# Performance work log

Hardware: AMD Instinct MI355X
Metric: run time of the kernel (lower is better)

The kernel has to match this reference:

```python
import jax, jax.numpy as jnp
import numpy as np

L, H, S, HID, E, TOPK = 2, 8, 1024, 512, 8, 2
FFN = 2 * HID
EPS = 1e-5


def setup_inputs() -> dict:
    key = jax.random.key(0)
    ks = jax.random.split(key, 20)
    B = 4
    sc = 0.02
    inp = {
        'x': jax.random.normal(ks[0], (B, S, HID), jnp.float32),
        'encoder_output': jax.random.normal(ks[1], (B, S, HID), jnp.float32),
        # two attentions per layer -> axis 1 of size 2 (0: masked self-attn, 1: cross-attn)
        'attn_wq': jax.random.normal(ks[2], (L, 2, HID, H * HID), jnp.float32) * sc,
        'attn_bq': jnp.zeros((L, 2, H * HID), jnp.float32),
        'attn_wk': jax.random.normal(ks[3], (L, 2, HID, H * HID), jnp.float32) * sc,
        'attn_bk': jnp.zeros((L, 2, H * HID), jnp.float32),
        'attn_wv': jax.random.normal(ks[4], (L, 2, HID, H * HID), jnp.float32) * sc,
        'attn_bv': jnp.zeros((L, 2, H * HID), jnp.float32),
        'attn_wo': jax.random.normal(ks[5], (L, 2, H * HID, HID), jnp.float32) * sc,
        'attn_bo': jnp.zeros((L, 2, HID), jnp.float32),
        'gate_w': jax.random.normal(ks[6], (L, HID, E), jnp.float32) * sc,
        'gate_b': jnp.zeros((L, E), jnp.float32),
        'exp_w1': jax.random.normal(ks[7], (L, E, HID, FFN), jnp.float32) * sc,
        'exp_b1': jnp.zeros((L, E, FFN), jnp.float32),
        'exp_w2': jax.random.normal(ks[8], (L, E, FFN, HID), jnp.float32) * sc,
        'exp_b2': jnp.zeros((L, E, HID), jnp.float32),
        'ln_g': jnp.ones((L, 3, HID), jnp.float32),
        'ln_b': jnp.zeros((L, 3, HID), jnp.float32),
    }
    return inp


def _layernorm(x, g, b):
    m = jnp.mean(x, -1, keepdims=True)
    v = jnp.mean(jnp.square(x - m), -1, keepdims=True)
    return g * (x - m) * jax.lax.rsqrt(v + EPS) + b


def _mha(q_in, k_in, v_in, wq, bq, wk, bk, wv, bv, wo, bo, masked):
    B = q_in.shape[0]
    # torch .view(-1, H, S, h) on [B, S, H*h]: raw memory reshape (faithful quirk)
    q = (q_in @ wq + bq).reshape(B, H, S, HID)
    k = (k_in @ wk + bk).reshape(B, H, S, HID)
    v = (v_in @ wv + bv).reshape(B, H, S, HID)
    scores = jnp.einsum('bhqd,bhkd->bhqk', q, k)  # d_k=1 -> scale = 1.0
    if masked:
        causal = jnp.triu(jnp.ones((S, S), jnp.float32), k=1)
        scores = jnp.where(causal == 1, -jnp.inf, scores)
    attn = jax.nn.softmax(scores, axis=-1)  # dropout off (eval)
    out = jnp.einsum('bhqk,bhkd->bhqd', attn, v)
    out = out.transpose(0, 2, 1, 3).reshape(B, S, H * HID)
    return out @ wo + bo


def _moe(x, gw, gb, w1, b1, w2, b2):
    gate = jax.nn.softmax(x @ gw + gb, axis=-1)  # [B,S,E]
    topw, topi = jax.lax.top_k(gate, TOPK)
    topw = topw / jnp.sum(topw, -1, keepdims=True)
    # faithful bug: the torch loop overwrites, so only k = TOPK-1 survives
    sel = topi[..., TOPK - 1]  # [B,S]
    wsel = topw[..., TOPK - 1]  # [B,S]
    y = jnp.zeros_like(x)
    for e in range(E):
        he = jax.nn.relu(x @ w1[e] + b1[e]) @ w2[e] + b2[e]
        y = y + jnp.where((sel == e)[..., None], he, 0.0)
    return y * wsel[..., None]


def reference(x, encoder_output, attn_wq, attn_bq, attn_wk, attn_bk, attn_wv,
              attn_bv, attn_wo, attn_bo, gate_w, gate_b, exp_w1, exp_b1,
              exp_w2, exp_b2, ln_g, ln_b):
    for l in range(L):
        a = _mha(x, x, x,
                 attn_wq[l, 0], attn_bq[l, 0], attn_wk[l, 0], attn_bk[l, 0],
                 attn_wv[l, 0], attn_bv[l, 0], attn_wo[l, 0], attn_bo[l, 0],
                 masked=True)
        x = _layernorm(a + x, ln_g[l, 0], ln_b[l, 0])
        # cross-attn: query & key from encoder, values from x (faithful to source)
        a2 = _mha(encoder_output, encoder_output, x,
                  attn_wq[l, 1], attn_bq[l, 1], attn_wk[l, 1], attn_bk[l, 1],
                  attn_wv[l, 1], attn_bv[l, 1], attn_wo[l, 1], attn_bo[l, 1],
                  masked=False)
        x = _layernorm(x + a2, ln_g[l, 1], ln_b[l, 1])
        f = _moe(x, gate_w[l], gate_b[l], exp_w1[l], exp_b1[l], exp_w2[l], exp_b2[l])
        x = _layernorm(x + f, ln_g[l, 2], ln_b[l, 2])
    return x
```

## Files before the change

### kernel.cpp

```cpp
#include <hip/hip_runtime.h>
#include <math.h>


typedef unsigned short bf16_t;
typedef __attribute__((ext_vector_type(8))) short s16x8;
typedef __attribute__((ext_vector_type(8))) unsigned short u16x8;
typedef __attribute__((ext_vector_type(4))) float f32x4;

__device__ __forceinline__ float bf2f(bf16_t u) {
    union { unsigned int i; float f; } v; v.i = ((unsigned int)u) << 16; return v.f;
}
__device__ __forceinline__ bf16_t f2bf(float f) {
    union { float f; unsigned int i; } v; v.f = f;
    unsigned int x = v.i;
    return (bf16_t)((x + 0x7fffu + ((x >> 16) & 1u)) >> 16);
}
__device__ __forceinline__ bf16_t bfhi_trunc(float x, float& rem) {
    union { float f; unsigned u; } v; v.f = x;
    unsigned hu = v.u & 0xFFFF0000u;
    union { unsigned u; float f; } h; h.u = hu;
    rem = x - h.f;
    return (bf16_t)(hu >> 16);
}

__device__ __forceinline__ float waveReduceSum(float x) {
    x += __shfl_xor(x, 1);  x += __shfl_xor(x, 2);  x += __shfl_xor(x, 4);
    x += __shfl_xor(x, 8);  x += __shfl_xor(x, 16); x += __shfl_xor(x, 32);
    return x;
}
__device__ __forceinline__ float waveReduceMax(float x) {
    x = fmaxf(x, __shfl_xor(x, 1));  x = fmaxf(x, __shfl_xor(x, 2));
    x = fmaxf(x, __shfl_xor(x, 4));  x = fmaxf(x, __shfl_xor(x, 8));
    x = fmaxf(x, __shfl_xor(x, 16)); x = fmaxf(x, __shfl_xor(x, 32));
    return x;
}

__global__ void probe_kernel(const unsigned int* __restrict__ lng_u32,
                             int* __restrict__ flag)
{
    if (threadIdx.x == 0 && blockIdx.x == 0)
        *flag = (lng_u32[0] == 0x3F803F80u) ? 1 : 0;
}


__device__ __forceinline__ void stage_f32_row(const float* __restrict__ src,
                                              char* rowp, int h, int r)
{
    float xx[16];
    *(float4*)(xx + 0)  = *(const float4*)(src + 0);
    *(float4*)(xx + 4)  = *(const float4*)(src + 4);
    *(float4*)(xx + 8)  = *(const float4*)(src + 8);
    *(float4*)(xx + 12) = *(const float4*)(src + 12);
    u16x8 h0, h1, l0, l1;
#pragma unroll
    for (int i = 0; i < 8; i++) {
        float r0, r1;
        h0[i] = bfhi_trunc(xx[i], r0);      l0[i] = f2bf(r0);
        h1[i] = bfhi_trunc(xx[8 + i], r1);  l1[i] = f2bf(r1);
    }
    const int sw = (r & 7) << 4;
    *(u16x8*)(rowp + ((32 * h + 0)  ^ sw)) = h0;
    *(u16x8*)(rowp + ((32 * h + 16) ^ sw)) = h1;
    *(u16x8*)(rowp + ((64 + 32 * h + 0)  ^ sw)) = l0;
    *(u16x8*)(rowp + ((64 + 32 * h + 16) ^ sw)) = l1;
}

__device__ __forceinline__ void stage_bf16_row(const bf16_t* __restrict__ src,
                                               char* rowp, int h, int r)
{
    u16x8 v0 = *(const u16x8*)(src);
    u16x8 v1 = *(const u16x8*)(src + 8);
    const int sw = (r & 7) << 4;
    *(u16x8*)(rowp + ((32 * h + 0)  ^ sw)) = v0;
    *(u16x8*)(rowp + ((32 * h + 16) ^ sw)) = v1;
}

__device__ __forceinline__ void stage_wnn_bf16(const bf16_t* __restrict__ src,
                                               int ldb, ushort (*Bs)[64],
                                               int kp2, int n8)
{
    u16x8 r0 = *(const u16x8*)(src);
    u16x8 r1 = *(const u16x8*)(src + ldb);
#pragma unroll
    for (int j = 0; j < 8; j++) {
        int rr = n8 + j;
        unsigned v = (unsigned)(unsigned short)r0[j] |
                     ((unsigned)(unsigned short)r1[j] << 16);
        *(unsigned*)((char*)&Bs[rr][0] + ((2 * kp2) ^ ((rr & 7) << 4))) = v;
    }
}

__device__ __forceinline__ void stage_wnn_f32(const float* __restrict__ src,
                                              int ldb, ushort (*Bs)[64],
                                              int kp2, int n8)
{
    float a0[8], a1[8];
    *(float4*)(a0 + 0) = *(const float4*)(src);
    *(float4*)(a0 + 4) = *(const float4*)(src + 4);
    *(float4*)(a1 + 0) = *(const float4*)(src + ldb);
    *(float4*)(a1 + 4) = *(const float4*)(src + ldb + 4);
#pragma unroll
    for (int j = 0; j < 8; j++) {
        int rr = n8 + j;
        float q0, q1;
        bf16_t h0 = bfhi_trunc(a0[j], q0);
        bf16_t h1 = bfhi_trunc(a1[j], q1);
        unsigned vh = (unsigned)h0 | ((unsigned)h1 << 16);
        unsigned vl = (unsigned)f2bf(q0) | ((unsigned)f2bf(q1) << 16);
        char* rp = (char*)&Bs[rr][0];
        int sw = (rr & 7) << 4;
        *(unsigned*)(rp + ((2 * kp2) ^ sw)) = vh;
        *(unsigned*)(rp + ((64 + 2 * kp2) ^ sw)) = vl;
    }
}

template<bool NT, bool RELU, bool GATHER, bool SCALE>
__device__ __forceinline__
void mgemm_body(const float* __restrict__ aF, const bf16_t* __restrict__ aH,
                const bool aBf,
                const float* __restrict__ bF, const bf16_t* __restrict__ bH,
                const bool bBf,
                const float* __restrict__ biasF, const bf16_t* __restrict__ biasH,
                const bool bf, const bool hasb,
                float* __restrict__ Cp,
                int lda, int ldb, int ldc,
                int Meff, const int* __restrict__ gl,
                const float* __restrict__ scalev,
                int kBeg, int kEnd, int m0, int n0)
{
    __shared__ __align__(16) ushort As[128][64];
    __shared__ __align__(16) ushort Bs[128][64];

    const int t   = threadIdx.x;
    const int sr  = t >> 1;
    const int sh  = t & 1;
    const int kp2 = (t & 15) * 2;
    const int n8  = (t >> 4) * 8;

    int agr = m0 + sr;
    if (GATHER) agr = gl[(m0 + sr < Meff) ? (m0 + sr) : (Meff - 1)];

    const int lane = t & 63;
    const int wv = t >> 6;
    const int wr = wv >> 1, wc = wv & 1;
    const int lr = lane & 15, kg = lane >> 4;

    int aoffH[4], aoffL[4], boffH[4], boffL[4];
#pragma unroll
    for (int i = 0; i < 4; i++) {
        int ra = wr * 64 + i * 16 + lr;
        int sa = (ra & 7) << 4;
        aoffH[i] = ra * 128 + ((kg * 16) ^ sa);
        aoffL[i] = ra * 128 + ((64 + kg * 16) ^ sa);
        int rb = wc * 64 + i * 16 + lr;
        int sb = (rb & 7) << 4;
        boffH[i] = rb * 128 + ((kg * 16) ^ sb);
        boffL[i] = rb * 128 + ((64 + kg * 16) ^ sb);
    }

    f32x4 acc[4][4];
#pragma unroll
    for (int i = 0; i < 4; i++)
#pragma unroll
        for (int j = 0; j < 4; j++)
            acc[i][j] = (f32x4){0.f, 0.f, 0.f, 0.f};

    for (int k0 = kBeg; k0 < kEnd; k0 += 32) {
        __syncthreads();
        {
            char* rowp = (char*)&As[sr][0];
            if (aBf) stage_bf16_row(aH + (long)agr * lda + k0 + sh * 16, rowp, sh, sr);
            else     stage_f32_row (aF + (long)agr * lda + k0 + sh * 16, rowp, sh, sr);
        }
        if (NT) {
            char* rowp = (char*)&Bs[sr][0];
            stage_f32_row(bF + (long)(n0 + sr) * ldb + k0 + sh * 16, rowp, sh, sr);
        } else if (bBf) {
            stage_wnn_bf16(bH + (long)(k0 + kp2) * ldb + n0 + n8, ldb, Bs, kp2, n8);
        } else {
            stage_wnn_f32 (bF + (long)(k0 + kp2) * ldb + n0 + n8, ldb, Bs, kp2, n8);
        }
        __syncthreads();

        s16x8 aHi[4], aLo[4];
#pragma unroll
        for (int i = 0; i < 4; i++)
            aHi[i] = *(const s16x8*)((const char*)As + aoffH[i]);
        if (!aBf) {
#pragma unroll
            for (int i = 0; i < 4; i++)
                aLo[i] = *(const s16x8*)((const char*)As + aoffL[i]);
        }

#pragma unroll
        for (int j = 0; j < 4; j++) {
            s16x8 bHi = *(const s16x8*)((const char*)Bs + boffH[j]);
#pragma unroll
            for (int i = 0; i < 4; i++)
                acc[i][j] = __builtin_amdgcn_mfma_f32_16x16x32_bf16(
                    aHi[i], bHi, acc[i][j], 0, 0, 0);
            if (!bBf) {
                s16x8 bLo = *(const s16x8*)((const char*)Bs + boffL[j]);
#pragma unroll
                for (int i = 0; i < 4; i++)
                    acc[i][j] = __builtin_amdgcn_mfma_f32_16x16x32_bf16(
                        aHi[i], bLo, acc[i][j], 0, 0, 0);
            }
            if (!aBf) {
#pragma unroll
                for (int i = 0; i < 4; i++)
                    acc[i][j] = __builtin_amdgcn_mfma_f32_16x16x32_bf16(
                        aLo[i], bHi, acc[i][j], 0, 0, 0);
            }
        }
    }

#pragma unroll
    for (int j = 0; j < 4; j++) {
        int col = n0 + wc * 64 + j * 16 + lr;
        float bv = 0.f;
        if (hasb) bv = bf ? bf2f(biasH[col]) : biasF[col];
#pragma unroll
        for (int i = 0; i < 4; i++) {
#pragma unroll
            for (int rr = 0; rr < 4; rr++) {
                int grow = m0 + wr * 64 + i * 16 + kg * 4 + rr;
                if (GATHER && grow >= Meff) continue;
                int crow = GATHER ? gl[grow] : grow;
                float v = acc[i][j][rr] + bv;
                if (RELU) v = fmaxf(v, 0.f);
                if (SCALE) v *= scalev[crow];
                Cp[(long)crow * ldc + col] = v;
            }
        }
    }
}

template<bool A_INPUT, bool B_WEIGHT, bool NT, bool RELU, bool GATHER,
         bool SCALE, bool MASK_TRI, bool MASK_K, bool SPLITK>
__global__ __launch_bounds__(256, 2)
void mgemm_kernel(const void* a32, const void* a16,
                  const void* b32, const void* b16,
                  const void* bias32, const void* bias16,
                  float* __restrict__ C,
                  int M, int N, int K, int lda, int ldb, int ldc,
                  long aZ, long bZ, long biasZ, long cZ,
                  const int* __restrict__ glist, const int* __restrict__ counts,
                  const float* __restrict__ scalev,
                  const int* __restrict__ dtf)
{
    if (MASK_TRI && blockIdx.x > blockIdx.y) return;
    const int e  = SPLITK ? 0 : blockIdx.z;
    const int n0 = blockIdx.x * 128, m0 = blockIdx.y * 128;
    int Meff = M;
    const int* gl = nullptr;
    if (GATHER) {
        gl = glist + e * 4096;
        Meff = counts[e];
        if (m0 >= Meff) return;
    }
    const bool bf  = (*dtf != 0);
    const bool aBf = A_INPUT && bf;
    const bool bBf = B_WEIGHT && bf;

    const float*  aF = (const float*)a32 + (long)e * aZ;
    const bf16_t* aH = (const bf16_t*)a16 + (long)e * aZ;
    const long bOff  = SPLITK ? 0 : (long)e * bZ;
    const float*  bF = (const float*)b32 + bOff;
    const bf16_t* bH = (const bf16_t*)b16 + bOff;

    float* Cp;
    int kBeg = 0, kEnd = K;
    if (SPLITK) {
        const int kc  = blockIdx.z;
        const int kch = (int)bZ;
        kBeg = kc * kch;
        kEnd = kBeg + kch;
        Cp = C + (long)kc * cZ;
    } else {
        Cp = C + (long)e * cZ;
        if (MASK_K) kEnd = (blockIdx.y + 1) * 128;
    }
    const bool hasb = !SPLITK && ((bias32 != nullptr) || (bias16 != nullptr));
    const float*  biasF = (const float*)bias32 + (long)e * biasZ;
    const bf16_t* biasH = (const bf16_t*)bias16 + (long)e * biasZ;

    mgemm_body<NT, RELU, GATHER, SCALE>(aF, aH, aBf, bF, bH, bBf,
        biasF, biasH, bf, hasb, Cp, lda, ldb, ldc, Meff, gl, scalev,
        kBeg, kEnd, m0, n0);
}

struct TriArgs {
    const void* a32[3]; const void* a16[3];
    const void* w32[3]; const void* w16[3];
    const void* b32[3]; const void* b16[3];
    float* dst[3];
    int aIn[3];
};

__global__ __launch_bounds__(256, 2)
void mgemm_tri_kernel(TriArgs ta, int lda, int ldb, int ldc, int K,
                      const int* __restrict__ dtf)
{
    const int z  = blockIdx.z;
    const int n0 = blockIdx.x * 128, m0 = blockIdx.y * 128;
    const bool bf  = (*dtf != 0);
    const bool aBf = (ta.aIn[z] != 0) && bf;
    mgemm_body<false, false, false, false>(
        (const float*)ta.a32[z], (const bf16_t*)ta.a16[z], aBf,
        (const float*)ta.w32[z], (const bf16_t*)ta.w16[z], bf,
        (const float*)ta.b32[z], (const bf16_t*)ta.b16[z], bf, true,
        ta.dst[z], lda, ldb, ldc, 0, nullptr, nullptr,
        0, K, m0, n0);
}

template<int NCH>
__global__ __launch_bounds__(256)
void reduce_kernel(const float* __restrict__ part,
                   const void* bias32, const void* bias16,
                   float* __restrict__ out, const int* __restrict__ dtf)
{
    const bool bf = (*dtf != 0);
    const int i = (blockIdx.x * 256 + threadIdx.x) * 4;
    float4 s = *(const float4*)(part + i);
#pragma unroll
    for (int c = 1; c < NCH; c++) {
        float4 p = *(const float4*)(part + (long)c * 524288 + i);
        s.x += p.x; s.y += p.y; s.z += p.z; s.w += p.w;
    }
    const int col = i & 511;
    float b0, b1, b2, b3;
    if (bf) {
        const bf16_t* bb = (const bf16_t*)bias16;
        b0 = bf2f(bb[col]); b1 = bf2f(bb[col + 1]);
        b2 = bf2f(bb[col + 2]); b3 = bf2f(bb[col + 3]);
    } else {
        const float* bb = (const float*)bias32;
        b0 = bb[col]; b1 = bb[col + 1]; b2 = bb[col + 2]; b3 = bb[col + 3];
    }
    out[i + 0] = s.x + b0; out[i + 1] = s.y + b1;
    out[i + 2] = s.z + b2; out[i + 3] = s.w + b3;
}

template<bool MASKED>
__global__ __launch_bounds__(256)
void softmax_kernel(float* __restrict__ sb)
{
    const int g = blockIdx.x * 4 + (threadIdx.x >> 6);
    const int lane = threadIdx.x & 63;
    const int r = g & 1023;
    float* row = sb + (long)g * 1024;
    const int n = MASKED ? (r + 1) : 1024;

    float vv[16];
    float m = -1e30f;
#pragma unroll
    for (int j = 0; j < 4; j++) {
        float4 v4 = *(const float4*)(row + j * 256 + lane * 4);
        const float* pv = (const float*)&v4;
#pragma unroll
        for (int c = 0; c < 4; c++) {
            int idx = j * 256 + lane * 4 + c;
            float x = (idx < n) ? pv[c] : -1e30f;
            vv[j * 4 + c] = x;
            m = fmaxf(m, x);
        }
    }
    m = waveReduceMax(m);
    float sum = 0.0f;
#pragma unroll
    for (int i = 0; i < 16; i++) {
        vv[i] = __expf(vv[i] - m);
        sum += vv[i];
    }
    sum = waveReduceSum(sum);
    float inv = 1.0f / sum;
#pragma unroll
    for (int j = 0; j < 4; j++) {
        float4 o = make_float4(vv[j * 4 + 0] * inv, vv[j * 4 + 1] * inv,
                               vv[j * 4 + 2] * inv, vv[j * 4 + 3] * inv);
        *(float4*)(row + j * 256 + lane * 4) = o;
    }
}

template<bool MASKED>
__global__ __launch_bounds__(256)
void flash_kernel(const float* __restrict__ q, const float* __restrict__ k,
                  const float* __restrict__ v, float* __restrict__ outc)
{
    const int h = blockIdx.y;
    const long bh = (long)h * 524288L;
    q += bh; k += bh; v += bh;
    const int t = threadIdx.x, lane = t & 63, wave = t >> 6;
    const int base = blockIdx.x * 32;
    const int row0 = base + wave * 8;

    float qreg[8][8], oacc[8][8];
    float mi[8], li[8];
#pragma unroll
    for (int i = 0; i < 8; i++) {
        mi[i] = -1e30f;
        li[i] = 0.0f;
#pragma unroll
        for (int d = 0; d < 8; d++) {
            qreg[i][d] = q[(long)(row0 + i) * 512 + lane + 64 * d];
            oacc[i][d] = 0.0f;
        }
    }

    __shared__ float ks[8][512];
    __shared__ float vs[8][512];

    const int kmax = MASKED ? (base + 31) : 1023;
    for (int k0 = 0; k0 <= kmax; k0 += 8) {
        __syncthreads();
#pragma unroll
        for (int r = 0; r < 4; r++) {
            int flat = (r * 256 + t) * 4;
            int kr = flat >> 9, col = flat & 511;
            *(float4*)&ks[kr][col] = *(const float4*)&k[(long)(k0 + kr) * 512 + col];
            *(float4*)&vs[kr][col] = *(const float4*)&v[(long)(k0 + kr) * 512 + col];
        }
        __syncthreads();
#pragma unroll
        for (int j = 0; j < 8; j++) {
            const int kg = k0 + j;
#pragma unroll
            for (int i = 0; i < 8; i++) {
                const int qrow = row0 + i;
                if (MASKED && kg > qrow) continue;
                float p = 0.0f;
#pragma unroll
                for (int d = 0; d < 8; d++)
                    p = fmaf(qreg[i][d], ks[j][lane + 64 * d], p);
                p = waveReduceSum(p);
                float mnew = fmaxf(mi[i], p);
                float sc = __expf(mi[i] - mnew);
                float pe = __expf(p - mnew);
                li[i] = li[i] * sc + pe;
                mi[i] = mnew;
#pragma unroll
                for (int d = 0; d < 8; d++)
                    oacc[i][d] = fmaf(oacc[i][d], sc, pe * vs[j][lane + 64 * d]);
            }
        }
    }

#pragma unroll
    for (int i = 0; i < 8; i++) {
        float inv = 1.0f / li[i];
        long off = (long)(row0 + i) * 4096 + h * 512 + lane;
#pragma unroll
        for (int d = 0; d < 8; d++)
            outc[off + 64 * d] = oacc[i][d] * inv;
    }
}

template<bool R_WS, bool O_WS>
__global__ __launch_bounds__(256)
void add_ln_kernel(const float* __restrict__ a,
                   const void* r32, const void* r16,
                   const void* g32, const void* g16,
                   const void* b32, const void* b16,
                   void* out, const int* __restrict__ dtf)
{
    const bool bf = (*dtf != 0);
    const int row = blockIdx.x, t = threadIdx.x;
    const long o = (long)row * 512;

    float r0, r1;
    if (R_WS) {
        r0 = ((const float*)r32)[o + t];
        r1 = ((const float*)r32)[o + 256 + t];
    } else if (bf) {
        r0 = bf2f(((const bf16_t*)r16)[o + t]);
        r1 = bf2f(((const bf16_t*)r16)[o + 256 + t]);
    } else {
        r0 = ((const float*)r32)[o + t];
        r1 = ((const float*)r32)[o + 256 + t];
    }
    float z0 = a[o + t] + r0;
    float z1 = a[o + 256 + t] + r1;

    __shared__ float red[4];
    const int lane = t & 63, wave = t >> 6;

    float s = waveReduceSum(z0 + z1);
    if (lane == 0) red[wave] = s;
    __syncthreads();
    float mean = (red[0] + red[1] + red[2] + red[3]) * (1.0f / 512.0f);
    float d0 = z0 - mean, d1 = z1 - mean;
    float vsum = waveReduceSum(d0 * d0 + d1 * d1);
    __syncthreads();
    if (lane == 0) red[wave] = vsum;
    __syncthreads();
    float var = (red[0] + red[1] + red[2] + red[3]) * (1.0f / 512.0f);
    float rstd = rsqrtf(var + 1e-5f);

    float gg0, gg1, bb0, bb1;
    if (bf) {
        gg0 = bf2f(((const bf16_t*)g16)[t]);  gg1 = bf2f(((const bf16_t*)g16)[t + 256]);
        bb0 = bf2f(((const bf16_t*)b16)[t]);  bb1 = bf2f(((const bf16_t*)b16)[t + 256]);
    } else {
        gg0 = ((const float*)g32)[t];         gg1 = ((const float*)g32)[t + 256];
        bb0 = ((const float*)b32)[t];         bb1 = ((const float*)b32)[t + 256];
    }
    float o0 = gg0 * d0 * rstd + bb0;
    float o1 = gg1 * d1 * rstd + bb1;
    if (O_WS) {
        ((float*)out)[o + t] = o0;
        ((float*)out)[o + 256 + t] = o1;
    } else if (bf) {
        ((bf16_t*)out)[o + t] = f2bf(o0);
        ((bf16_t*)out)[o + 256 + t] = f2bf(o1);
    } else {
        ((float*)out)[o + t] = o0;
        ((float*)out)[o + 256 + t] = o1;
    }
}

__global__ __launch_bounds__(256)
void gate_kernel(const float* __restrict__ x,
                 const void* gw32, const void* gw16,
                 const void* gb32, const void* gb16,
                 int* __restrict__ sel, float* __restrict__ wsel,
                 const int* __restrict__ dtf)
{
    const bool bf = (*dtf != 0);
    const int lane = threadIdx.x & 63, wave = threadIdx.x >> 6;
    const int token = blockIdx.x * 4 + wave;
    float xr[8];
#pragma unroll
    for (int i = 0; i < 8; i++) xr[i] = x[(long)token * 512 + lane + 64 * i];
    float logits[8];
#pragma unroll
    for (int e = 0; e < 8; e++) {
        float p = 0.0f;
#pragma unroll
        for (int i = 0; i < 8; i++) {
            long idx = (long)(lane + 64 * i) * 8 + e;
            float w = bf ? bf2f(((const bf16_t*)gw16)[idx]) : ((const float*)gw32)[idx];
            p = fmaf(xr[i], w, p);
        }
        p = waveReduceSum(p);
        float b = bf ? bf2f(((const bf16_t*)gb16)[e]) : ((const float*)gb32)[e];
        logits[e] = p + b;
    }
    if (lane == 0) {
        float m1 = -1e30f, m2 = -1e30f;
        int i1 = 0, i2 = 0;
#pragma unroll
        for (int e = 0; e < 8; e++) {
            float vv = logits[e];
            if (vv > m1) { m2 = m1; i2 = i1; m1 = vv; i1 = e; }
            else if (vv > m2) { m2 = vv; i2 = e; }
        }
        float ed = __expf(m2 - m1);
        sel[token]  = i2;
        wsel[token] = ed / (1.0f + ed);
    }
}

__global__ void zero_counts_kernel(int* __restrict__ counts)
{
    if (threadIdx.x < 8) counts[threadIdx.x] = 0;
}

__global__ __launch_bounds__(256)
void route_kernel(const int* __restrict__ sel, int* __restrict__ counts,
                  int* __restrict__ idx)
{
    int tk = blockIdx.x * 256 + threadIdx.x;
    int e = sel[tk] & 7;
    int pos = atomicAdd(&counts[e], 1) & 4095;
    idx[e * 4096 + pos] = tk;
}

extern "C" void kernel_launch(void* const* d_in, const int* in_sizes, int n_in,
                              void* d_out, int out_size, void* d_ws, size_t ws_size,
                              hipStream_t stream)
{
    const char* x_in = (const char*)d_in[0];
    const char* enc  = (const char*)d_in[1];
    const char* wq   = (const char*)d_in[2];
    const char* bq   = (const char*)d_in[3];
    const char* wk   = (const char*)d_in[4];
    const char* bk   = (const char*)d_in[5];
    const char* wv   = (const char*)d_in[6];
    const char* bv   = (const char*)d_in[7];
    const char* wo   = (const char*)d_in[8];
    const char* bo   = (const char*)d_in[9];
    const char* gw   = (const char*)d_in[10];
    const char* gb   = (const char*)d_in[11];
    const char* ew1  = (const char*)d_in[12];
    const char* eb1  = (const char*)d_in[13];
    const char* ew2  = (const char*)d_in[14];
    const char* eb2  = (const char*)d_in[15];
    const char* lng  = (const char*)d_in[16];
    const char* lnb  = (const char*)d_in[17];

    float* ws = (float*)d_ws;
    const long SZ_X = 4096L * 512;
    const long SZ_B = 1024L * 4096;
    float* xb = ws;
    float* ab = xb + SZ_X;
    float* qb = ab + SZ_X;
    float* kb = qb + SZ_B;
    float* vb = kb + SZ_B;
    float* cb = vb + SZ_B;
    float* h1 = qb;
    float* yb = kb;
    float* wselp = cb + SZ_B;
    int* selp   = (int*)(wselp + 4096);
    int* counts = selp + 4096;
    int* idxl   = counts + 8;
    int* dtf    = idxl + 8 * 4096;
    long sb_off = (((long)(dtf + 1 - (int*)ws)) + 3) & ~3L;
    float* sbuf = ws + sb_off;
    const long NEED = (sb_off + 8L * 1048576L) * 4L;
    const bool big = (ws_size >= (size_t)NEED);

    dim3 blk(256);
    const long SB = 1024L * 512;
    const long L3 = 512L * 4096;
    const long LO = 4096L * 512;

    probe_kernel<<<1, 64, 0, stream>>>((const unsigned int*)lng, dtf);

    const char* cur = x_in;
    bool cur_is_ws = false;

    for (int l = 0; l < 2; l++) {
        for (int att = 0; att < 2; att++) {
            const long woff = (long)(l * 2 + att);
            const void* Wx32[4] = { wq + woff * L3 * 4, wk + woff * L3 * 4,
                                    wv + woff * L3 * 4, wo + woff * LO * 4 };
            const void* Wx16[4] = { wq + woff * L3 * 2, wk + woff * L3 * 2,
                                    wv + woff * L3 * 2, wo + woff * LO * 2 };
            const void* Bx32[4] = { bq + woff * 4096 * 4, bk + woff * 4096 * 4,
                                    bv + woff * 4096 * 4, bo + woff * 512 * 4 };
            const void* Bx16[4] = { bq + woff * 4096 * 2, bk + woff * 4096 * 2,
                                    bv + woff * 4096 * 2, bo + woff * 512 * 2 };

            for (int b = 0; b < 4; b++) {
                const char* Aqk = (att == 1) ? enc : cur;
                const bool  aqk_in = (att == 1) || !cur_is_ws;
                float* dst3[3] = { qb, kb, vb };

                TriArgs ta;
                for (int m = 0; m < 3; m++) {
                    const char* Asrc = (m == 2) ? cur : Aqk;
                    const bool  a_in = (m == 2) ? !cur_is_ws : aqk_in;
                    ta.a32[m] = Asrc + b * SB * 4;
                    ta.a16[m] = Asrc + b * SB * 2;
                    ta.aIn[m] = a_in ? 1 : 0;
                    ta.w32[m] = Wx32[m]; ta.w16[m] = Wx16[m];
                    ta.b32[m] = Bx32[m]; ta.b16[m] = Bx16[m];
                    ta.dst[m] = dst3[m];
                }
                mgemm_tri_kernel<<<dim3(32, 8, 3), blk, 0, stream>>>(
                    ta, 512, 4096, 4096, 512, dtf);

                if (big) {
                    if (att == 0) {
                        mgemm_kernel<false, false, true, false, false, false, true, false, false>
                            <<<dim3(8, 8, 8), blk, 0, stream>>>(
                            qb, nullptr, kb, nullptr, nullptr, nullptr, sbuf,
                            1024, 1024, 512, 512, 512, 1024,
                            524288L, 524288L, 0, 1048576L,
                            nullptr, nullptr, nullptr, dtf);
                        softmax_kernel<true><<<2048, blk, 0, stream>>>(sbuf);
                        mgemm_kernel<false, false, false, false, false, false, false, true, false>
                            <<<dim3(4, 8, 8), blk, 0, stream>>>(
                            sbuf, nullptr, vb, nullptr, nullptr, nullptr, cb,
                            1024, 512, 1024, 1024, 512, 4096,
                            1048576L, 524288L, 0, 512L,
                            nullptr, nullptr, nullptr, dtf);
                    } else {
                        mgemm_kernel<false, false, true, false, false, false, false, false, false>
                            <<<dim3(8, 8, 8), blk, 0, stream>>>(
                            qb, nullptr, kb, nullptr, nullptr, nullptr, sbuf,
                            1024, 1024, 512, 512, 512, 1024,
                            524288L, 524288L, 0, 1048576L,
                            nullptr, nullptr, nullptr, dtf);
                        softmax_kernel<false><<<2048, blk, 0, stream>>>(sbuf);
                        mgemm_kernel<false, false, false, false, false, false, false, false, false>
                            <<<dim3(4, 8, 8), blk, 0, stream>>>(
                            sbuf, nullptr, vb, nullptr, nullptr, nullptr, cb,
                            1024, 512, 1024, 1024, 512, 4096,
                            1048576L, 524288L, 0, 512L,
                            nullptr, nullptr, nullptr, dtf);
                    }
                    mgemm_kernel<false, true, false, false, false, false, false, false, true>
                        <<<dim3(4, 8, 16), blk, 0, stream>>>(
                        cb, nullptr, Wx32[3], Wx16[3], nullptr, nullptr, sbuf,
                        1024, 512, 4096, 4096, 512, 512,
                        0, 256 , 0, 524288L ,
                        nullptr, nullptr, nullptr, dtf);
                    reduce_kernel<16><<<512, blk, 0, stream>>>(
                        sbuf, Bx32[3], Bx16[3], ab + b * SB, dtf);
                } else {
                    if (att == 0)
                        flash_kernel<true><<<dim3(32, 8), blk, 0, stream>>>(qb, kb, vb, cb);
                    else
                        flash_kernel<false><<<dim3(32, 8), blk, 0, stream>>>(qb, kb, vb, cb);
                    mgemm_kernel<false, true, false, false, false, false, false, false, false>
                        <<<dim3(4, 8, 1), blk, 0, stream>>>(
                        cb, nullptr, Wx32[3], Wx16[3], Bx32[3], Bx16[3], ab + b * SB,
                        1024, 512, 4096, 4096, 512, 512,
                        0, 0, 0, 0, nullptr, nullptr, nullptr, dtf);
                }
            }

            const void* G32  = lng + (long)(l * 3 + att) * 512 * 4;
            const void* G16  = lng + (long)(l * 3 + att) * 512 * 2;
            const void* Bt32 = lnb + (long)(l * 3 + att) * 512 * 4;
            const void* Bt16 = lnb + (long)(l * 3 + att) * 512 * 2;
            if (cur_is_ws)
                add_ln_kernel<true, true><<<4096, blk, 0, stream>>>(
                    ab, (const void*)cur, nullptr, G32, G16, Bt32, Bt16, xb, dtf);
            else
                add_ln_kernel<false, true><<<4096, blk, 0, stream>>>(
                    ab, (const void*)cur, (const void*)cur, G32, G16, Bt32, Bt16, xb, dtf);
            cur = (const char*)xb; cur_is_ws = true;
        }

        gate_kernel<<<1024, blk, 0, stream>>>(
            xb, gw + (long)l * 512 * 8 * 4, gw + (long)l * 512 * 8 * 2,
            gb + (long)l * 8 * 4, gb + (long)l * 8 * 2, selp, wselp, dtf);
        zero_counts_kernel<<<1, 64, 0, stream>>>(counts);
        route_kernel<<<16, blk, 0, stream>>>(selp, counts, idxl);

        mgemm_kernel<false, true, false, true, true, false, false, false, false>
            <<<dim3(8, 32, 8), blk, 0, stream>>>(
            xb, nullptr,
            ew1 + (long)l * 8 * 512 * 1024 * 4, ew1 + (long)l * 8 * 512 * 1024 * 2,
            eb1 + (long)l * 8 * 1024 * 4, eb1 + (long)l * 8 * 1024 * 2, h1,
            4096, 1024, 512, 512, 1024, 1024,
            0, 512L * 1024, 1024, 0, idxl, counts, nullptr, dtf);
        mgemm_kernel<false, true, false, false, true, true, false, false, false>
            <<<dim3(4, 32, 8), blk, 0, stream>>>(
            h1, nullptr,
            ew2 + (long)l * 8 * 1024 * 512 * 4, ew2 + (long)l * 8 * 1024 * 512 * 2,
            eb2 + (long)l * 8 * 512 * 4, eb2 + (long)l * 8 * 512 * 2, yb,
            4096, 512, 1024, 1024, 512, 512,
            0, 1024L * 512, 512, 0, idxl, counts, wselp, dtf);

        const void* G32  = lng + (long)(l * 3 + 2) * 512 * 4;
        const void* G16  = lng + (long)(l * 3 + 2) * 512 * 2;
        const void* Bt32 = lnb + (long)(l * 3 + 2) * 512 * 4;
        const void* Bt16 = lnb + (long)(l * 3 + 2) * 512 * 2;
        if (l == 0)
            add_ln_kernel<true, true><<<4096, blk, 0, stream>>>(
                yb, (const void*)xb, nullptr, G32, G16, Bt32, Bt16, xb, dtf);
        else
            add_ln_kernel<true, false><<<4096, blk, 0, stream>>>(
                yb, (const void*)xb, nullptr, G32, G16, Bt32, Bt16, d_out, dtf);
    }
}
```

Before: 4.001 ms.

## Store intermediate activations as pre-split bf16 hi/lo pairs instead of fp32

Intermediate buffers (x, Q/K/V, softmax probabilities, attention context, expert hidden) are now written as two bf16 planes (round-to-nearest hi plus residual lo) instead of fp32. GEMM staging loads these pairs directly rather than reading fp32 and splitting per tile, which removes repeated conversion work and keeps memory traffic the same. This adds split work in the epilogues and extra kernel plumbing through modes, and it changes the split rounding from truncation to round-to-nearest.

```diff
diff --git a/kernel.cpp b/kernel.cpp
--- a/kernel.cpp
+++ b/kernel.cpp
@@ -22,6 +22,12 @@
     rem = x - h.f;
     return (bf16_t)(hu >> 16);
 }
+__device__ __forceinline__ void split_rne(float x, bf16_t& hi, bf16_t& lo) {
+    bf16_t h = f2bf(x);
+    float hf = bf2f(h);
+    lo = f2bf(x - hf);
+    hi = h;
+}
 
 __device__ __forceinline__ float waveReduceSum(float x) {
     x += __shfl_xor(x, 1);  x += __shfl_xor(x, 2);  x += __shfl_xor(x, 4);
@@ -75,9 +81,24 @@
     *(u16x8*)(rowp + ((32 * h + 16) ^ sw)) = v1;
 }
 
+__device__ __forceinline__ void stage_pair_row(const bf16_t* __restrict__ hi,
+                                               const bf16_t* __restrict__ lo,
+                                               char* rowp, int h, int r)
+{
+    u16x8 h0 = *(const u16x8*)(hi);
+    u16x8 h1 = *(const u16x8*)(hi + 8);
+    u16x8 l0 = *(const u16x8*)(lo);
+    u16x8 l1 = *(const u16x8*)(lo + 8);
+    const int sw = (r & 7) << 4;
+    *(u16x8*)(rowp + ((32 * h + 0)  ^ sw)) = h0;
+    *(u16x8*)(rowp + ((32 * h + 16) ^ sw)) = h1;
+    *(u16x8*)(rowp + ((64 + 32 * h + 0)  ^ sw)) = l0;
+    *(u16x8*)(rowp + ((64 + 32 * h + 16) ^ sw)) = l1;
+}
+
 __device__ __forceinline__ void stage_wnn_bf16(const bf16_t* __restrict__ src,
                                                int ldb, ushort (*Bs)[64],
-                                               int kp2, int n8)
+                                               int kp2, int n8, int base)
 {
     u16x8 r0 = *(const u16x8*)(src);
     u16x8 r1 = *(const u16x8*)(src + ldb);
@@ -86,7 +107,7 @@
         int rr = n8 + j;
         unsigned v = (unsigned)(unsigned short)r0[j] |
                      ((unsigned)(unsigned short)r1[j] << 16);
-        *(unsigned*)((char*)&Bs[rr][0] + ((2 * kp2) ^ ((rr & 7) << 4))) = v;
+        *(unsigned*)((char*)&Bs[rr][0] + ((base + 2 * kp2) ^ ((rr & 7) << 4))) = v;
     }
 }
 
@@ -114,15 +135,15 @@
     }
 }
 
-template<bool NT, bool RELU, bool GATHER, bool SCALE>
+template<bool NT, bool RELU, bool GATHER, bool SCALE, bool OUTP>
 __device__ __forceinline__
-void mgemm_body(const float* __restrict__ aF, const bf16_t* __restrict__ aH,
-                const bool aBf,
-                const float* __restrict__ bF, const bf16_t* __restrict__ bH,
-                const bool bBf,
+void mgemm_body(int am, const float* __restrict__ aF,
+                const bf16_t* __restrict__ aH, const bf16_t* __restrict__ aL,
+                int bm, const float* __restrict__ bF,
+                const bf16_t* __restrict__ bH, const bf16_t* __restrict__ bL,
                 const float* __restrict__ biasF, const bf16_t* __restrict__ biasH,
                 const bool bf, const bool hasb,
-                float* __restrict__ Cp,
+                float* __restrict__ Cp, bf16_t* __restrict__ CpH, long cplane,
                 int lda, int ldb, int ldc,
                 int Meff, const int* __restrict__ gl,
                 const float* __restrict__ scalev,
@@ -165,20 +186,34 @@
         for (int j = 0; j < 4; j++)
             acc[i][j] = (f32x4){0.f, 0.f, 0.f, 0.f};
 
+    const bool aHasLo = (am != 1);
+    const bool bHasLo = (bm != 1);
+
     for (int k0 = kBeg; k0 < kEnd; k0 += 32) {
         __syncthreads();
         {
             char* rowp = (char*)&As[sr][0];
-            if (aBf) stage_bf16_row(aH + (long)agr * lda + k0 + sh * 16, rowp, sh, sr);
-            else     stage_f32_row (aF + (long)agr * lda + k0 + sh * 16, rowp, sh, sr);
+            long aoff = (long)agr * lda + k0 + sh * 16;
+            if (am == 2)      stage_pair_row(aH + aoff, aL + aoff, rowp, sh, sr);
+            else if (am == 1) stage_bf16_row(aH + aoff, rowp, sh, sr);
+            else              stage_f32_row (aF + aoff, rowp, sh, sr);
         }
         if (NT) {
             char* rowp = (char*)&Bs[sr][0];
-            stage_f32_row(bF + (long)(n0 + sr) * ldb + k0 + sh * 16, rowp, sh, sr);
-        } else if (bBf) {
-            stage_wnn_bf16(bH + (long)(k0 + kp2) * ldb + n0 + n8, ldb, Bs, kp2, n8);
+            long boff = (long)(n0 + sr) * ldb + k0 + sh * 16;
+            if (bm == 2)      stage_pair_row(bH + boff, bL + boff, rowp, sh, sr);
+            else if (bm == 1) stage_bf16_row(bH + boff, rowp, sh, sr);
+            else              stage_f32_row (bF + boff, rowp, sh, sr);
         } else {
-            stage_wnn_f32 (bF + (long)(k0 + kp2) * ldb + n0 + n8, ldb, Bs, kp2, n8);
+            long boff = (long)(k0 + kp2) * ldb + n0 + n8;
+            if (bm == 2) {
+                stage_wnn_bf16(bH + boff, ldb, Bs, kp2, n8, 0);
+                stage_wnn_bf16(bL + boff, ldb, Bs, kp2, n8, 64);
+            } else if (bm == 1) {
+                stage_wnn_bf16(bH + boff, ldb, Bs, kp2, n8, 0);
+            } else {
+                stage_wnn_f32 (bF + boff, ldb, Bs, kp2, n8);
+            }
         }
         __syncthreads();
 
@@ -186,7 +221,7 @@
 #pragma unroll
         for (int i = 0; i < 4; i++)
             aHi[i] = *(const s16x8*)((const char*)As + aoffH[i]);
-        if (!aBf) {
+        if (aHasLo) {
 #pragma unroll
             for (int i = 0; i < 4; i++)
                 aLo[i] = *(const s16x8*)((const char*)As + aoffL[i]);
@@ -199,14 +234,14 @@
             for (int i = 0; i < 4; i++)
                 acc[i][j] = __builtin_amdgcn_mfma_f32_16x16x32_bf16(
                     aHi[i], bHi, acc[i][j], 0, 0, 0);
-            if (!bBf) {
+            if (bHasLo) {
                 s16x8 bLo = *(const s16x8*)((const char*)Bs + boffL[j]);
 #pragma unroll
                 for (int i = 0; i < 4; i++)
                     acc[i][j] = __builtin_amdgcn_mfma_f32_16x16x32_bf16(
                         aHi[i], bLo, acc[i][j], 0, 0, 0);
             }
-            if (!aBf) {
+            if (aHasLo) {
 #pragma unroll
                 for (int i = 0; i < 4; i++)
                     acc[i][j] = __builtin_amdgcn_mfma_f32_16x16x32_bf16(
@@ -230,19 +265,28 @@
                 float v = acc[i][j][rr] + bv;
                 if (RELU) v = fmaxf(v, 0.f);
                 if (SCALE) v *= scalev[crow];
-                Cp[(long)crow * ldc + col] = v;
+                if (OUTP) {
+                    bf16_t hh, ll;
+                    split_rne(v, hh, ll);
+                    long off = (long)crow * ldc + col;
+                    CpH[off] = hh;
+                    CpH[cplane + off] = ll;
+                } else {
+                    Cp[(long)crow * ldc + col] = v;
+                }
             }
         }
     }
 }
 
-template<bool A_INPUT, bool B_WEIGHT, bool NT, bool RELU, bool GATHER,
-         bool SCALE, bool MASK_TRI, bool MASK_K, bool SPLITK>
+template<bool NT, bool RELU, bool GATHER, bool SCALE,
+         bool MASK_TRI, bool MASK_K, bool SPLITK, bool OUTP>
 __global__ __launch_bounds__(256, 2)
-void mgemm_kernel(const void* a32, const void* a16,
-                  const void* b32, const void* b16,
+void mgemm_kernel(int amode, int bmode,
+                  const void* a32, const void* a16, const void* a16lo,
+                  const void* b32, const void* b16, const void* b16lo,
                   const void* bias32, const void* bias16,
-                  float* __restrict__ C,
+                  float* C, void* CH, long cplane,
                   int M, int N, int K, int lda, int ldb, int ldc,
                   long aZ, long bZ, long biasZ, long cZ,
                   const int* __restrict__ glist, const int* __restrict__ counts,
@@ -259,17 +303,20 @@
         Meff = counts[e];
         if (m0 >= Meff) return;
     }
-    const bool bf  = (*dtf != 0);
-    const bool aBf = A_INPUT && bf;
-    const bool bBf = B_WEIGHT && bf;
+    const bool bf = (*dtf != 0);
+    const int am = (amode < 0) ? (bf ? 1 : 0) : amode;
+    const int bm = (bmode < 0) ? (bf ? 1 : 0) : bmode;
 
     const float*  aF = (const float*)a32 + (long)e * aZ;
     const bf16_t* aH = (const bf16_t*)a16 + (long)e * aZ;
+    const bf16_t* aL = (const bf16_t*)a16lo + (long)e * aZ;
     const long bOff  = SPLITK ? 0 : (long)e * bZ;
     const float*  bF = (const float*)b32 + bOff;
     const bf16_t* bH = (const bf16_t*)b16 + bOff;
-
-    float* Cp;
+    const bf16_t* bL = (const bf16_t*)b16lo + bOff;
+
+    float* Cp = nullptr;
+    bf16_t* CpH = nullptr;
     int kBeg = 0, kEnd = K;
     if (SPLITK) {
         const int kc  = blockIdx.z;
@@ -278,40 +325,43 @@
         kEnd = kBeg + kch;
         Cp = C + (long)kc * cZ;
     } else {
-        Cp = C + (long)e * cZ;
+        if (C)  Cp  = C + (long)e * cZ;
+        if (CH) CpH = (bf16_t*)CH + (long)e * cZ;
         if (MASK_K) kEnd = (blockIdx.y + 1) * 128;
     }
     const bool hasb = !SPLITK && ((bias32 != nullptr) || (bias16 != nullptr));
     const float*  biasF = (const float*)bias32 + (long)e * biasZ;
     const bf16_t* biasH = (const bf16_t*)bias16 + (long)e * biasZ;
 
-    mgemm_body<NT, RELU, GATHER, SCALE>(aF, aH, aBf, bF, bH, bBf,
-        biasF, biasH, bf, hasb, Cp, lda, ldb, ldc, Meff, gl, scalev,
-        kBeg, kEnd, m0, n0);
+    mgemm_body<NT, RELU, GATHER, SCALE, OUTP>(am, aF, aH, aL, bm, bF, bH, bL,
+        biasF, biasH, bf, hasb, Cp, CpH, cplane, lda, ldb, ldc, Meff, gl,
+        scalev, kBeg, kEnd, m0, n0);
 }
 
 struct TriArgs {
-    const void* a32[3]; const void* a16[3];
+    const void* aF[3]; const void* aH[3]; const void* aL[3];
     const void* w32[3]; const void* w16[3];
     const void* b32[3]; const void* b16[3];
-    float* dst[3];
-    int aIn[3];
+    void* dstH[3];
+    int am[3];
 };
 
 __global__ __launch_bounds__(256, 2)
-void mgemm_tri_kernel(TriArgs ta, int lda, int ldb, int ldc, int K,
-                      const int* __restrict__ dtf)
-{
-    const int z  = blockIdx.z;
-    const int n0 = blockIdx.x * 128, m0 = blockIdx.y * 128;
-    const bool bf  = (*dtf != 0);
-    const bool aBf = (ta.aIn[z] != 0) && bf;
-    mgemm_body<false, false, false, false>(
-        (const float*)ta.a32[z], (const bf16_t*)ta.a16[z], aBf,
-        (const float*)ta.w32[z], (const bf16_t*)ta.w16[z], bf,
-        (const float*)ta.b32[z], (const bf16_t*)ta.b16[z], bf, true,
-        ta.dst[z], lda, ldb, ldc, 0, nullptr, nullptr,
-        0, K, m0, n0);
+void mgemm_tri_kernel(TriArgs ta, const int* __restrict__ dtf)
+{
+    const int z = blockIdx.z;
+    const bool bf = (*dtf != 0);
+    const int am = (ta.am[z] < 0) ? (bf ? 1 : 0) : ta.am[z];
+    const int bm = bf ? 1 : 0;
+    mgemm_body<false, false, false, false, true>(
+        am, (const float*)ta.aF[z], (const bf16_t*)ta.aH[z], (const bf16_t*)ta.aL[z],
+        bm, (const float*)ta.w32[z], (const bf16_t*)ta.w16[z], nullptr,
+        (const float*)ta.b32[z], (const bf16_t*)ta.b16[z],
+        bf, true,
+        nullptr, (bf16_t*)ta.dstH[z], 4194304L,
+        512, 4096, 4096,
+        0, nullptr, nullptr,
+        0, 512, blockIdx.y * 128, blockIdx.x * 128);
 }
 
 template<int NCH>
@@ -350,6 +400,7 @@
     const int lane = threadIdx.x & 63;
     const int r = g & 1023;
     float* row = sb + (long)g * 1024;
+    bf16_t* rowh = (bf16_t*)row;
     const int n = MASKED ? (r + 1) : 1024;
 
     float vv[16];
@@ -377,20 +428,28 @@
     float inv = 1.0f / sum;
 #pragma unroll
     for (int j = 0; j < 4; j++) {
-        float4 o = make_float4(vv[j * 4 + 0] * inv, vv[j * 4 + 1] * inv,
-                               vv[j * 4 + 2] * inv, vv[j * 4 + 3] * inv);
-        *(float4*)(row + j * 256 + lane * 4) = o;
+        ushort4 hh, ll;
+        float p0 = vv[j * 4 + 0] * inv, p1 = vv[j * 4 + 1] * inv;
+        float p2 = vv[j * 4 + 2] * inv, p3 = vv[j * 4 + 3] * inv;
+        bf16_t h, l;
+        split_rne(p0, h, l); hh.x = h; ll.x = l;
+        split_rne(p1, h, l); hh.y = h; ll.y = l;
+        split_rne(p2, h, l); hh.z = h; ll.z = l;
+        split_rne(p3, h, l); hh.w = h; ll.w = l;
+        *(ushort4*)(rowh + (j * 256 + lane * 4)) = hh;
+        *(ushort4*)(rowh + 1024 + (j * 256 + lane * 4)) = ll;
     }
 }
 
 template<bool MASKED>
 __global__ __launch_bounds__(256)
-void flash_kernel(const float* __restrict__ q, const float* __restrict__ k,
-                  const float* __restrict__ v, float* __restrict__ outc)
+void flash_kernel(const bf16_t* __restrict__ qh, const bf16_t* __restrict__ ql,
+                  const bf16_t* __restrict__ kh, const bf16_t* __restrict__ kl,
+                  const bf16_t* __restrict__ vh, const bf16_t* __restrict__ vl,
+                  bf16_t* __restrict__ outH)
 {
     const int h = blockIdx.y;
     const long bh = (long)h * 524288L;
-    q += bh; k += bh; v += bh;
     const int t = threadIdx.x, lane = t & 63, wave = t >> 6;
     const int base = blockIdx.x * 32;
     const int row0 = base + wave * 8;
@@ -403,7 +462,8 @@
         li[i] = 0.0f;
 #pragma unroll
         for (int d = 0; d < 8; d++) {
-            qreg[i][d] = q[(long)(row0 + i) * 512 + lane + 64 * d];
+            long idx = bh + (long)(row0 + i) * 512 + lane + 64 * d;
+            qreg[i][d] = bf2f(qh[idx]) + bf2f(ql[idx]);
             oacc[i][d] = 0.0f;
         }
     }
@@ -418,8 +478,19 @@
         for (int r = 0; r < 4; r++) {
             int flat = (r * 256 + t) * 4;
             int kr = flat >> 9, col = flat & 511;
-            *(float4*)&ks[kr][col] = *(const float4*)&k[(long)(k0 + kr) * 512 + col];
-            *(float4*)&vs[kr][col] = *(const float4*)&v[(long)(k0 + kr) * 512 + col];
+            long idx = bh + (long)(k0 + kr) * 512 + col;
+            ushort4 kh4 = *(const ushort4*)&kh[idx];
+            ushort4 kl4 = *(const ushort4*)&kl[idx];
+            ushort4 vh4 = *(const ushort4*)&vh[idx];
+            ushort4 vl4 = *(const ushort4*)&vl[idx];
+            ks[kr][col + 0] = bf2f(kh4.x) + bf2f(kl4.x);
+            ks[kr][col + 1] = bf2f(kh4.y) + bf2f(kl4.y);
+            ks[kr][col + 2] = bf2f(kh4.z) + bf2f(kl4.z);
+            ks[kr][col + 3] = bf2f(kh4.w) + bf2f(kl4.w);
+            vs[kr][col + 0] = bf2f(vh4.x) + bf2f(vl4.x);
+            vs[kr][col + 1] = bf2f(vh4.y) + bf2f(vl4.y);
+            vs[kr][col + 2] = bf2f(vh4.z) + bf2f(vl4.z);
+            vs[kr][col + 3] = bf2f(vh4.w) + bf2f(vl4.w);
         }
         __syncthreads();
 #pragma unroll
@@ -449,29 +520,35 @@
 #pragma unroll
     for (int i = 0; i < 8; i++) {
         float inv = 1.0f / li[i];
-        long off = (long)(row0 + i) * 4096 + h * 512 + lane;
-#pragma unroll
-        for (int d = 0; d < 8; d++)
-            outc[off + 64 * d] = oacc[i][d] * inv;
-    }
-}
-
-template<bool R_WS, bool O_WS>
+#pragma unroll
+        for (int d = 0; d < 8; d++) {
+            long off = (long)(row0 + i) * 4096 + h * 512 + lane + 64 * d;
+            bf16_t hh, ll;
+            split_rne(oacc[i][d] * inv, hh, ll);
+            outH[off] = hh;
+            outH[4194304L + off] = ll;
+        }
+    }
+}
+
+template<int RM, int OM>
 __global__ __launch_bounds__(256)
 void add_ln_kernel(const float* __restrict__ a,
-                   const void* r32, const void* r16,
+                   const void* r32, const void* r16, const void* r16lo,
                    const void* g32, const void* g16,
                    const void* b32, const void* b16,
-                   void* out, const int* __restrict__ dtf)
+                   void* out, void* outLo, const int* __restrict__ dtf)
 {
     const bool bf = (*dtf != 0);
     const int row = blockIdx.x, t = threadIdx.x;
     const long o = (long)row * 512;
 
     float r0, r1;
-    if (R_WS) {
-        r0 = ((const float*)r32)[o + t];
-        r1 = ((const float*)r32)[o + 256 + t];
+    if (RM == 1) {
+        const bf16_t* rh = (const bf16_t*)r16;
+        const bf16_t* rl = (const bf16_t*)r16lo;
+        r0 = bf2f(rh[o + t]) + bf2f(rl[o + t]);
+        r1 = bf2f(rh[o + 256 + t]) + bf2f(rl[o + 256 + t]);
     } else if (bf) {
         r0 = bf2f(((const bf16_t*)r16)[o + t]);
         r1 = bf2f(((const bf16_t*)r16)[o + 256 + t]);
@@ -507,9 +584,12 @@
     }
     float o0 = gg0 * d0 * rstd + bb0;
     float o1 = gg1 * d1 * rstd + bb1;
-    if (O_WS) {
-        ((float*)out)[o + t] = o0;
-        ((float*)out)[o + 256 + t] = o1;
+    if (OM == 1) {
+        bf16_t* oh = (bf16_t*)out;
+        bf16_t* ol = (bf16_t*)outLo;
+        bf16_t hh, ll;
+        split_rne(o0, hh, ll); oh[o + t] = hh;        ol[o + t] = ll;
+        split_rne(o1, hh, ll); oh[o + 256 + t] = hh;  ol[o + 256 + t] = ll;
     } else if (bf) {
         ((bf16_t*)out)[o + t] = f2bf(o0);
         ((bf16_t*)out)[o + 256 + t] = f2bf(o1);
@@ -520,7 +600,7 @@
 }
 
 __global__ __launch_bounds__(256)
-void gate_kernel(const float* __restrict__ x,
+void gate_kernel(const bf16_t* __restrict__ xh, const bf16_t* __restrict__ xl,
                  const void* gw32, const void* gw16,
                  const void* gb32, const void* gb16,
                  int* __restrict__ sel, float* __restrict__ wsel,
@@ -531,7 +611,10 @@
     const int token = blockIdx.x * 4 + wave;
     float xr[8];
 #pragma unroll
-    for (int i = 0; i < 8; i++) xr[i] = x[(long)token * 512 + lane + 64 * i];
+    for (int i = 0; i < 8; i++) {
+        long idx = (long)token * 512 + lane + 64 * i;
+        xr[i] = bf2f(xh[idx]) + bf2f(xl[idx]);
+    }
     float logits[8];
 #pragma unroll
     for (int e = 0; e < 8; e++) {
@@ -620,6 +703,14 @@
     const long NEED = (sb_off + 8L * 1048576L) * 4L;
     const bool big = (ws_size >= (size_t)NEED);
 
+    bf16_t* xh  = (bf16_t*)xb;   bf16_t* xl  = xh + 2097152;
+    bf16_t* qh  = (bf16_t*)qb;   bf16_t* ql  = qh + 4194304;
+    bf16_t* kh  = (bf16_t*)kb;   bf16_t* kl  = kh + 4194304;
+    bf16_t* vh  = (bf16_t*)vb;   bf16_t* vl  = vh + 4194304;
+    bf16_t* cbh = (bf16_t*)cb;   bf16_t* cbl = cbh + 4194304;
+    bf16_t* h1h = (bf16_t*)h1;   bf16_t* h1l = h1h + 4194304;
+    bf16_t* sbh = (bf16_t*)sbuf;
+
     dim3 blk(256);
     const long SB = 1024L * 512;
     const long L3 = 512L * 4096;
@@ -643,57 +734,68 @@
                                     bv + woff * 4096 * 2, bo + woff * 512 * 2 };
 
             for (int b = 0; b < 4; b++) {
-                const char* Aqk = (att == 1) ? enc : cur;
-                const bool  aqk_in = (att == 1) || !cur_is_ws;
-                float* dst3[3] = { qb, kb, vb };
+                const bool aqk_in = (att == 1) || !cur_is_ws;
+                void* dst3[3] = { qb, kb, vb };
 
                 TriArgs ta;
                 for (int m = 0; m < 3; m++) {
-                    const char* Asrc = (m == 2) ? cur : Aqk;
-                    const bool  a_in = (m == 2) ? !cur_is_ws : aqk_in;
-                    ta.a32[m] = Asrc + b * SB * 4;
-                    ta.a16[m] = Asrc + b * SB * 2;
-                    ta.aIn[m] = a_in ? 1 : 0;
+                    const bool a_in = (m == 2) ? !cur_is_ws : aqk_in;
+                    if (a_in) {
+                        const char* Asrc = (m == 2) ? x_in : ((att == 1) ? enc : x_in);
+                        ta.am[m] = -1;
+                        ta.aF[m] = Asrc + b * SB * 4;
+                        ta.aH[m] = Asrc + b * SB * 2;
+                        ta.aL[m] = nullptr;
+                    } else {
+                        ta.am[m] = 2;
+                        ta.aF[m] = nullptr;
+                        ta.aH[m] = xh + b * SB;
+                        ta.aL[m] = xl + b * SB;
+                    }
                     ta.w32[m] = Wx32[m]; ta.w16[m] = Wx16[m];
                     ta.b32[m] = Bx32[m]; ta.b16[m] = Bx16[m];
-                    ta.dst[m] = dst3[m];
+                    ta.dstH[m] = dst3[m];
                 }
-                mgemm_tri_kernel<<<dim3(32, 8, 3), blk, 0, stream>>>(
-                    ta, 512, 4096, 4096, 512, dtf);
+                mgemm_tri_kernel<<<dim3(32, 8, 3), blk, 0, stream>>>(ta, dtf);
 
                 if (big) {
                     if (att == 0) {
-                        mgemm_kernel<false, false, true, false, false, false, true, false, false>
+                        mgemm_kernel<true, false, false, false, true, false, false, false>
                             <<<dim3(8, 8, 8), blk, 0, stream>>>(
-                            qb, nullptr, kb, nullptr, nullptr, nullptr, sbuf,
+                            2, 2, nullptr, qh, ql, nullptr, kh, kl,
+                            nullptr, nullptr, sbuf, nullptr, 0,
                             1024, 1024, 512, 512, 512, 1024,
                             524288L, 524288L, 0, 1048576L,
                             nullptr, nullptr, nullptr, dtf);
                         softmax_kernel<true><<<2048, blk, 0, stream>>>(sbuf);
-                        mgemm_kernel<false, false, false, false, false, false, false, true, false>
+                        mgemm_kernel<false, false, false, false, false, true, false, true>
                             <<<dim3(4, 8, 8), blk, 0, stream>>>(
-                            sbuf, nullptr, vb, nullptr, nullptr, nullptr, cb,
-                            1024, 512, 1024, 1024, 512, 4096,
-                            1048576L, 524288L, 0, 512L,
+                            2, 2, nullptr, sbh, sbh + 1024, nullptr, vh, vl,
+                            nullptr, nullptr, nullptr, cbh, 4194304L,
+                            1024, 512, 1024, 2048, 512, 4096,
+                            2097152L, 524288L, 0, 512L,
                             nullptr, nullptr, nullptr, dtf);
                     } else {
-                        mgemm_kernel<false, false, true, false, false, false, false, false, false>
+                        mgemm_kernel<true, false, false, false, false, false, false, false>
                             <<<dim3(8, 8, 8), blk, 0, stream>>>(
-                            qb, nullptr, kb, nullptr, nullptr, nullptr, sbuf,
+                            2, 2, nullptr, qh, ql, nullptr, kh, kl,
+                            nullptr, nullptr, sbuf, nullptr, 0,
                             1024, 1024, 512, 512, 512, 1024,
                             524288L, 524288L, 0, 1048576L,
                             nullptr, nullptr, nullptr, dtf);
                         softmax_kernel<false><<<2048, blk, 0, stream>>>(sbuf);
-                        mgemm_kernel<false, false, false, false, false, false, false, false, false>
+                        mgemm_kernel<false, false, false, false, false, false, false, true>
                             <<<dim3(4, 8, 8), blk, 0, stream>>>(
-                            sbuf, nullptr, vb, nullptr, nullptr, nullptr, cb,
-                            1024, 512, 1024, 1024, 512, 4096,
-                            1048576L, 524288L, 0, 512L,
+                            2, 2, nullptr, sbh, sbh + 1024, nullptr, vh, vl,
+                            nullptr, nullptr, nullptr, cbh, 4194304L,
+                            1024, 512, 1024, 2048, 512, 4096,
+                            2097152L, 524288L, 0, 512L,
                             nullptr, nullptr, nullptr, dtf);
                     }
-                    mgemm_kernel<false, true, false, false, false, false, false, false, true>
+                    mgemm_kernel<false, false, false, false, false, false, true, false>
                         <<<dim3(4, 8, 16), blk, 0, stream>>>(
-                        cb, nullptr, Wx32[3], Wx16[3], nullptr, nullptr, sbuf,
+                        2, -1, nullptr, cbh, cbl, Wx32[3], Wx16[3], nullptr,
+                        nullptr, nullptr, sbuf, nullptr, 0,
                         1024, 512, 4096, 4096, 512, 512,
                         0, 256 , 0, 524288L ,
                         nullptr, nullptr, nullptr, dtf);
@@ -701,12 +803,15 @@
                         sbuf, Bx32[3], Bx16[3], ab + b * SB, dtf);
                 } else {
                     if (att == 0)
-                        flash_kernel<true><<<dim3(32, 8), blk, 0, stream>>>(qb, kb, vb, cb);
+                        flash_kernel<true><<<dim3(32, 8), blk, 0, stream>>>(
+                            qh, ql, kh, kl, vh, vl, cbh);
                     else
-                        flash_kernel<false><<<dim3(32, 8), blk, 0, stream>>>(qb, kb, vb, cb);
-                    mgemm_kernel<false, true, false, false, false, false, false, false, false>
+                        flash_kernel<false><<<dim3(32, 8), blk, 0, stream>>>(
+                            qh, ql, kh, kl, vh, vl, cbh);
+                    mgemm_kernel<false, false, false, false, false, false, false, false>
                         <<<dim3(4, 8, 1), blk, 0, stream>>>(
-                        cb, nullptr, Wx32[3], Wx16[3], Bx32[3], Bx16[3], ab + b * SB,
+                        2, -1, nullptr, cbh, cbl, Wx32[3], Wx16[3], nullptr,
+                        Bx32[3], Bx16[3], ab + b * SB, nullptr, 0,
                         1024, 512, 4096, 4096, 512, 512,
                         0, 0, 0, 0, nullptr, nullptr, nullptr, dtf);
                 }
@@ -717,32 +822,37 @@
             const void* Bt32 = lnb + (long)(l * 3 + att) * 512 * 4;
             const void* Bt16 = lnb + (long)(l * 3 + att) * 512 * 2;
             if (cur_is_ws)
-                add_ln_kernel<true, true><<<4096, blk, 0, stream>>>(
-                    ab, (const void*)cur, nullptr, G32, G16, Bt32, Bt16, xb, dtf);
+                add_ln_kernel<1, 1><<<4096, blk, 0, stream>>>(
+                    ab, nullptr, xh, xl, G32, G16, Bt32, Bt16, xh, xl, dtf);
             else
-                add_ln_kernel<false, true><<<4096, blk, 0, stream>>>(
-                    ab, (const void*)cur, (const void*)cur, G32, G16, Bt32, Bt16, xb, dtf);
+                add_ln_kernel<0, 1><<<4096, blk, 0, stream>>>(
+                    ab, (const void*)cur, (const void*)cur, nullptr,
+                    G32, G16, Bt32, Bt16, xh, xl, dtf);
             cur = (const char*)xb; cur_is_ws = true;
         }
 
         gate_kernel<<<1024, blk, 0, stream>>>(
-            xb, gw + (long)l * 512 * 8 * 4, gw + (long)l * 512 * 8 * 2,
+            xh, xl, gw + (long)l * 512 * 8 * 4, gw + (long)l * 512 * 8 * 2,
             gb + (long)l * 8 * 4, gb + (long)l * 8 * 2, selp, wselp, dtf);
         zero_counts_kernel<<<1, 64, 0, stream>>>(counts);
         route_kernel<<<16, blk, 0, stream>>>(selp, counts, idxl);
 
-        mgemm_kernel<false, true, false, true, true, false, false, false, false>
+        mgemm_kernel<false, true, true, false, false, false, false, true>
             <<<dim3(8, 32, 8), blk, 0, stream>>>(
-            xb, nullptr,
+            2, -1, nullptr, xh, xl,
             ew1 + (long)l * 8 * 512 * 1024 * 4, ew1 + (long)l * 8 * 512 * 1024 * 2,
-            eb1 + (long)l * 8 * 1024 * 4, eb1 + (long)l * 8 * 1024 * 2, h1,
+            nullptr,
+            eb1 + (long)l * 8 * 1024 * 4, eb1 + (long)l * 8 * 1024 * 2,
+            nullptr, h1h, 4194304L,
             4096, 1024, 512, 512, 1024, 1024,
             0, 512L * 1024, 1024, 0, idxl, counts, nullptr, dtf);
-        mgemm_kernel<false, true, false, false, true, true, false, false, false>
+        mgemm_kernel<false, false, true, true, false, false, false, false>
             <<<dim3(4, 32, 8), blk, 0, stream>>>(
-            h1, nullptr,
+            2, -1, nullptr, h1h, h1l,
             ew2 + (long)l * 8 * 1024 * 512 * 4, ew2 + (long)l * 8 * 1024 * 512 * 2,
-            eb2 + (long)l * 8 * 512 * 4, eb2 + (long)l * 8 * 512 * 2, yb,
+            nullptr,
+            eb2 + (long)l * 8 * 512 * 4, eb2 + (long)l * 8 * 512 * 2,
+            yb, nullptr, 0,
             4096, 512, 1024, 1024, 512, 512,
             0, 1024L * 512, 512, 0, idxl, counts, wselp, dtf);
 
@@ -751,10 +861,10 @@
         const void* Bt32 = lnb + (long)(l * 3 + 2) * 512 * 4;
         const void* Bt16 = lnb + (long)(l * 3 + 2) * 512 * 2;
         if (l == 0)
-            add_ln_kernel<true, true><<<4096, blk, 0, stream>>>(
-                yb, (const void*)xb, nullptr, G32, G16, Bt32, Bt16, xb, dtf);
+            add_ln_kernel<1, 1><<<4096, blk, 0, stream>>>(
+                yb, nullptr, xh, xl, G32, G16, Bt32, Bt16, xh, xl, dtf);
         else
-            add_ln_kernel<true, false><<<4096, blk, 0, stream>>>(
-                yb, (const void*)xb, nullptr, G32, G16, Bt32, Bt16, d_out, dtf);
-    }
-}
+            add_ln_kernel<1, 0><<<4096, blk, 0, stream>>>(
+                yb, nullptr, xh, xl, G32, G16, Bt32, Bt16, d_out, nullptr, dtf);
+    }
+}
```

Result: slower. 4.295 ms (+7.3%).
